# Kernel optimization log

Hardware: AMD Instinct MI355X
Metric: run time of the kernel (lower is better)

The kernel has to match this reference:

```python
import jax, jax.numpy as jnp
import numpy as np


def setup_inputs() -> dict:
    key = jax.random.key(0)
    k1, = jax.random.split(key, 1)
    inputs = jax.random.normal(k1, (16, 64, 64, 512), dtype=jnp.float32)
    gamma = jnp.zeros((1,), dtype=jnp.float32)
    return {"inputs": inputs, "gamma": gamma}


def reference(inputs, gamma):
    # inputs: [B, H, W, C] (NHWC)
    B, H, W, C = inputs.shape
    vec_a = inputs.reshape(B, H * W, C)              # [B, N, C], N = H*W
    # channel Gram matrix: aTa[b, i, j] = sum_n a[b, n, i] * a[b, n, j]
    aTa = jnp.einsum('bni,bnj->bij', vec_a, vec_a)    # [B, C, C]
    attn = jax.nn.softmax(aTa, axis=-1)               # softmax over last axis
    # aaTa = attn @ vec_a^T -> [B, C, N]; transpose -> [B, N, C]
    aaTa = jnp.einsum('bij,bnj->bni', attn, vec_a)    # [B, N, C]
    aaTa = aaTa.reshape(B, H, W, C)
    return gamma * aaTa + inputs
```

## Files before the change

kernel.cpp:

```cpp
#include <hip/hip_runtime.h>

#define BATCH 16
#define NPIX  4096
#define CCH   512
#define NSPLIT 8
#define KSPL  (NPIX / NSPLIT)
#define NUT   10

using bf16x8   = __attribute__((ext_vector_type(8))) __bf16;
using floatx4  = __attribute__((ext_vector_type(4))) float;
using ushort8v = __attribute__((ext_vector_type(8))) unsigned short;
using ushort4v = __attribute__((ext_vector_type(4))) unsigned short;

static __device__ __forceinline__ unsigned short f2bf(float f) {
    unsigned u = __builtin_bit_cast(unsigned, f);
    unsigned r = 0x7fffu + ((u >> 16) & 1u);
    return (unsigned short)((u + r) >> 16);
}
static __device__ __forceinline__ float bf2f(unsigned short v) {
    unsigned u = ((unsigned)v) << 16;
    return __builtin_bit_cast(float, u);
}
static __device__ __forceinline__ void gld16(const unsigned short* g, unsigned short* l) {
    __builtin_amdgcn_global_load_lds(
        (const __attribute__((address_space(1))) void*)g,
        (__attribute__((address_space(3))) void*)l,
        16, 0, 0);
}
#define LOFF(p) ((unsigned)(unsigned long long)(__attribute__((address_space(3))) const void*)(p))
#define DSR(d, a, o) asm volatile("ds_read_b128 %0, %1 offset:" o : "=v"(d) : "v"(a))

__global__ __launch_bounds__(256) void k_cvt(const float* __restrict__ inp,
                                             unsigned short* __restrict__ Abf,
                                             unsigned short* __restrict__ AT) {
    __shared__ unsigned short sN[64 * 66];
    const int bn = blockIdx.x, bc = blockIdx.y, b = blockIdx.z;
    const int t  = threadIdx.x;
    const int n0 = bn * 64, c0 = bc * 64;
    const float* ip = inp + ((size_t)b * NPIX + n0) * CCH + c0;
    unsigned short* op = Abf + ((size_t)b * NPIX + n0) * CCH + c0;

#pragma unroll
    for (int r = 0; r < 2; ++r) {
        int n  = r * 32 + (t >> 3);
        int c8 = (t & 7) * 8;
        float4 v0 = *(const float4*)(ip + (size_t)n * CCH + c8);
        float4 v1 = *(const float4*)(ip + (size_t)n * CCH + c8 + 4);
        ushort8v w;
        w[0] = f2bf(v0.x); w[1] = f2bf(v0.y); w[2] = f2bf(v0.z); w[3] = f2bf(v0.w);
        w[4] = f2bf(v1.x); w[5] = f2bf(v1.y); w[6] = f2bf(v1.z); w[7] = f2bf(v1.w);
        *(ushort8v*)(op + (size_t)n * CCH + c8) = w;
        *(ushort8v*)&sN[n * 66 + c8] = w;
    }
    __syncthreads();

    const int cp = t >> 3;
    const int ng = (t & 7) * 8;
    ushort8v o0, o1;
#pragma unroll
    for (int k = 0; k < 8; ++k) {
        unsigned d = *(const unsigned*)&sN[(ng + k) * 66 + cp * 2];
        o0[k] = (unsigned short)(d & 0xffffu);
        o1[k] = (unsigned short)(d >> 16);
    }
    unsigned short* tp = AT + ((size_t)b * CCH + c0) * NPIX + n0;
    *(ushort8v*)(tp + (size_t)(cp * 2)     * NPIX + ng) = o0;
    *(ushort8v*)(tp + (size_t)(cp * 2 + 1) * NPIX + ng) = o1;
}

#define GEMM_COMP(AADR, BADR)                                                  \
    {                                                                          \
        bf16x8 af[2], bv[8];                                                   \
        DSR(af[0], (AADR), "0");    DSR(af[1], (AADR), "1024");                \
        DSR(bv[0], (BADR), "0");    DSR(bv[1], (BADR), "1024");                \
        DSR(bv[2], (BADR), "2048"); DSR(bv[3], (BADR), "3072");                \
        DSR(bv[4], (BADR), "4096"); DSR(bv[5], (BADR), "5120");                \
        DSR(bv[6], (BADR), "6144"); DSR(bv[7], (BADR), "7168");                \
        asm volatile("s_waitcnt lgkmcnt(0)" ::: "memory");                     \
        __builtin_amdgcn_sched_barrier(0);                                     \
        _Pragma("unroll")                                                      \
        for (int tm = 0; tm < 2; ++tm)                                         \
            _Pragma("unroll")                                                  \
            for (int tn = 0; tn < 8; ++tn)                                     \
                acc[tm][tn] = __builtin_amdgcn_mfma_f32_16x16x32_bf16(         \
                    af[tm], bv[tn], acc[tm][tn], 0, 0, 0);                     \
    }

#define GEMM_WAIT4                                                             \
    asm volatile("s_waitcnt vmcnt(4)" ::: "memory");                           \
    __builtin_amdgcn_s_barrier();
#define GEMM_WAIT0                                                             \
    asm volatile("s_waitcnt vmcnt(0)" ::: "memory");                           \
    __builtin_amdgcn_s_barrier();

__global__ __launch_bounds__(256) void k_ata(const unsigned short* __restrict__ AT,
                                             unsigned short* __restrict__ Sp) {
    __shared__ unsigned short sA0[128 * 32];
    __shared__ unsigned short sA1[128 * 32];
    __shared__ unsigned short sA2[128 * 32];
    __shared__ unsigned short sB0[128 * 32];
    __shared__ unsigned short sB1[128 * 32];
    __shared__ unsigned short sB2[128 * 32];
    const int u = blockIdx.x, s = blockIdx.y, b = blockIdx.z;
    const int ti = (u < 4) ? 0 : (u < 7) ? 1 : (u < 9) ? 2 : 3;
    const int u0 = ti * 5 - (ti * (ti + 1)) / 2;
    const int tj = ti + (u - u0);
    const unsigned short* pa = AT + ((size_t)b * CCH + ti * 128) * NPIX + s * KSPL;
    const unsigned short* pb = AT + ((size_t)b * CCH + tj * 128) * NPIX + s * KSPL;
    const int tid = threadIdx.x, lane = tid & 63, wave = tid >> 6;
    const int lrow = lane >> 2;
    const int lk   = (lane & 3) * 8;
    const int kq   = (lane >> 4) * 8;

    const unsigned aoff = (unsigned)((wave * 32 + (lane & 15)) * 64 + kq * 2);
    const unsigned boff = (unsigned)((lane & 15) * 64 + kq * 2);
    const unsigned aA0 = LOFF(sA0) + aoff, aA1 = LOFF(sA1) + aoff, aA2 = LOFF(sA2) + aoff;
    const unsigned aB0 = LOFF(sB0) + boff, aB1 = LOFF(sB1) + boff, aB2 = LOFF(sB2) + boff;

    floatx4 acc[2][8];
#pragma unroll
    for (int tm = 0; tm < 2; ++tm)
#pragma unroll
        for (int tn = 0; tn < 8; ++tn)
            acc[tm][tn] = floatx4{0.f, 0.f, 0.f, 0.f};

#define STG(DA, DB, K0)                                                        \
    {                                                                          \
        _Pragma("unroll")                                                      \
        for (int i = 0; i < 2; ++i) {                                          \
            const int r = wave * 32 + i * 16;                                  \
            gld16(pa + (size_t)(r + lrow) * NPIX + (K0) + lk, &DA[r * 32]);    \
            gld16(pb + (size_t)(r + lrow) * NPIX + (K0) + lk, &DB[r * 32]);    \
        }                                                                      \
    }
#define BODYS(NA, NB, K2, CA, CB) STG(NA, NB, K2) GEMM_COMP(CA, CB) GEMM_WAIT4

    STG(sA0, sB0, 0)
    STG(sA1, sB1, 32)
    GEMM_WAIT4

    BODYS(sA2, sB2,  64, aA0, aB0)
    BODYS(sA0, sB0,  96, aA1, aB1)
    BODYS(sA1, sB1, 128, aA2, aB2)
    BODYS(sA2, sB2, 160, aA0, aB0)
    BODYS(sA0, sB0, 192, aA1, aB1)
    BODYS(sA1, sB1, 224, aA2, aB2)
    BODYS(sA2, sB2, 256, aA0, aB0)
    BODYS(sA0, sB0, 288, aA1, aB1)
    BODYS(sA1, sB1, 320, aA2, aB2)
    BODYS(sA2, sB2, 352, aA0, aB0)
    BODYS(sA0, sB0, 384, aA1, aB1)
    BODYS(sA1, sB1, 416, aA2, aB2)
    BODYS(sA2, sB2, 448, aA0, aB0)
    BODYS(sA0, sB0, 480, aA1, aB1)
    GEMM_COMP(aA2, aB2) GEMM_WAIT0
    GEMM_COMP(aA0, aB0)
#undef BODYS
#undef STG

    unsigned short* Tb = Sp + ((((size_t)s * BATCH + b) * NUT + u) << 14);
#pragma unroll
    for (int tm = 0; tm < 2; ++tm)
#pragma unroll
        for (int tn = 0; tn < 8; ++tn) {
            ushort4v w;
#pragma unroll
            for (int r = 0; r < 4; ++r) w[r] = f2bf(acc[tm][tn][r]);
            *(ushort4v*)&Tb[((((wave * 2 + tm) * 8 + tn) * 64) + lane) * 4] = w;
        }
}

__global__ __launch_bounds__(256) void k_softmax(const unsigned short* __restrict__ Sp,
                                                 unsigned short* __restrict__ P) {
    __shared__ float red[6];
    const int row = blockIdx.x;
    const int b = row >> 9, i = row & 511;
    const int tid = threadIdx.x, lane = tid & 63, wave = tid >> 6;
    const size_t sstr = (size_t)BATCH * NUT * 16384;

    float x[2];
#pragma unroll
    for (int e = 0; e < 2; ++e) {
        const int j  = tid + e * 256;
        const int ti = i >> 7, tj = j >> 7;
        const int il = i & 127, jl = j & 127;
        const bool sw = ti > tj;
        const int a  = sw ? tj : ti;
        const int cm = sw ? ti : tj;
        const int u  = a * 4 + cm - ((a * (a + 1)) >> 1);
        const int rr = sw ? jl : il;
        const int cc = sw ? il : jl;
        const int off = ((((rr >> 4) * 8 + (cc >> 4)) * 64) +
                         ((rr >> 2) & 3) * 16 + (cc & 15)) * 4 + (rr & 3);
        const size_t base = (((size_t)b * NUT + u) << 14) + off;
        float v = 0.f;
#pragma unroll
        for (int s = 0; s < NSPLIT; ++s) v += bf2f(Sp[base + s * sstr]);
        x[e] = v;
    }

    float m = fmaxf(x[0], x[1]);
#pragma unroll
    for (int o = 32; o; o >>= 1) m = fmaxf(m, __shfl_xor(m, o, 64));
    if (lane == 0) red[wave] = m;
    __syncthreads();
    if (tid == 0) red[4] = fmaxf(fmaxf(red[0], red[1]), fmaxf(red[2], red[3]));
    __syncthreads();
    m = red[4];

    float e0 = __expf(x[0] - m), e1 = __expf(x[1] - m);
    float sum = e0 + e1;
#pragma unroll
    for (int o = 32; o; o >>= 1) sum += __shfl_xor(sum, o, 64);
    if (lane == 0) red[wave] = sum;
    __syncthreads();
    if (tid == 0) red[5] = red[0] + red[1] + red[2] + red[3];
    __syncthreads();
    float inv = 1.0f / red[5];

    P[(size_t)row * CCH + tid]       = f2bf(e0 * inv);
    P[(size_t)row * CCH + tid + 256] = f2bf(e1 * inv);
}

__global__ __launch_bounds__(512) void k_av(const unsigned short* __restrict__ Abf,
                                            const unsigned short* __restrict__ P,
                                            const float* __restrict__ inp,
                                            const float* __restrict__ gamma,
                                            float* __restrict__ out) {
    __shared__ unsigned short sA0[256 * 32];
    __shared__ unsigned short sA1[256 * 32];
    __shared__ unsigned short sA2[256 * 32];
    __shared__ unsigned short sB0[256 * 32];
    __shared__ unsigned short sB1[256 * 32];
    __shared__ unsigned short sB2[256 * 32];
    const int bn = blockIdx.x, bi = blockIdx.y, b = blockIdx.z;
    const unsigned short* pa = Abf + ((size_t)b * NPIX + bn * 256) * CCH;
    const unsigned short* pb = P + ((size_t)b * CCH + bi * 256) * CCH;
    const int tid = threadIdx.x, lane = tid & 63, wave = tid >> 6;
    const int wr = wave >> 2;
    const int wc = wave & 3;
    const int lrow = lane >> 2;
    const int lk   = (lane & 3) * 8;
    const int kq   = (lane >> 4) * 8;
    const float g = gamma[0];

    const unsigned aoff = (unsigned)((wr * 128 + (lane & 15)) * 64 + kq * 2);
    const unsigned boff = (unsigned)((wc * 64 + (lane & 15)) * 64 + kq * 2);
    const unsigned aA0 = LOFF(sA0) + aoff, aA1 = LOFF(sA1) + aoff, aA2 = LOFF(sA2) + aoff;
    const unsigned aB0 = LOFF(sB0) + boff, aB1 = LOFF(sB1) + boff, aB2 = LOFF(sB2) + boff;

    floatx4 acc[8][4];
#pragma unroll
    for (int m = 0; m < 8; ++m)
#pragma unroll
        for (int n = 0; n < 4; ++n)
            acc[m][n] = floatx4{0.f, 0.f, 0.f, 0.f};

#define STG(DA, DB, K0)                                                        \
    {                                                                          \
        _Pragma("unroll")                                                      \
        for (int i = 0; i < 2; ++i) {                                          \
            const int r = (wave * 2 + i) * 16;                                 \
            gld16(pa + (size_t)(r + lrow) * CCH + (K0) + lk, &DA[r * 32]);     \
            gld16(pb + (size_t)(r + lrow) * CCH + (K0) + lk, &DB[r * 32]);     \
        }                                                                      \
    }
#define AV_COMP(AADR, BADR)                                                    \
    {                                                                          \
        bf16x8 af[8], bv[4];                                                   \
        DSR(af[0], (AADR), "0");    DSR(af[1], (AADR), "1024");                \
        DSR(af[2], (AADR), "2048"); DSR(af[3], (AADR), "3072");                \
        DSR(af[4], (AADR), "4096"); DSR(af[5], (AADR), "5120");                \
        DSR(af[6], (AADR), "6144"); DSR(af[7], (AADR), "7168");                \
        DSR(bv[0], (BADR), "0");    DSR(bv[1], (BADR), "1024");                \
        DSR(bv[2], (BADR), "2048"); DSR(bv[3], (BADR), "3072");                \
        asm volatile("s_waitcnt lgkmcnt(0)" ::: "memory");                     \
        __builtin_amdgcn_sched_barrier(0);                                     \
        _Pragma("unroll")                                                      \
        for (int m = 0; m < 8; ++m)                                            \
            _Pragma("unroll")                                                  \
            for (int n = 0; n < 4; ++n)                                        \
                acc[m][n] = __builtin_amdgcn_mfma_f32_16x16x32_bf16(           \
                    af[m], bv[n], acc[m][n], 0, 0, 0);                         \
    }
#define BODYS(NA, NB, K2, CA, CB) STG(NA, NB, K2) AV_COMP(CA, CB) GEMM_WAIT4

    STG(sA0, sB0, 0)
    STG(sA1, sB1, 32)
    GEMM_WAIT4

    BODYS(sA2, sB2,  64, aA0, aB0)
    BODYS(sA0, sB0,  96, aA1, aB1)
    BODYS(sA1, sB1, 128, aA2, aB2)
    BODYS(sA2, sB2, 160, aA0, aB0)
    BODYS(sA0, sB0, 192, aA1, aB1)
    BODYS(sA1, sB1, 224, aA2, aB2)
    BODYS(sA2, sB2, 256, aA0, aB0)
    BODYS(sA0, sB0, 288, aA1, aB1)
    BODYS(sA1, sB1, 320, aA2, aB2)
    BODYS(sA2, sB2, 352, aA0, aB0)
    BODYS(sA0, sB0, 384, aA1, aB1)
    BODYS(sA1, sB1, 416, aA2, aB2)
    BODYS(sA2, sB2, 448, aA0, aB0)
    BODYS(sA0, sB0, 480, aA1, aB1)
    AV_COMP(aA2, aB2) GEMM_WAIT0
    AV_COMP(aA0, aB0)
#undef BODYS
#undef AV_COMP
#undef STG

    float* Ob = out + ((size_t)b * NPIX + bn * 256) * CCH + bi * 256;
    const float* Ib = inp + ((size_t)b * NPIX + bn * 256) * CCH + bi * 256;
#pragma unroll
    for (int m = 0; m < 8; ++m)
#pragma unroll
        for (int n = 0; n < 4; ++n)
#pragma unroll
            for (int r = 0; r < 4; ++r) {
                int nrow = wr * 128 + m * 16 + (lane >> 4) * 4 + r;
                int icol = wc * 64 + n * 16 + (lane & 15);
                size_t o = (size_t)nrow * CCH + icol;
                Ob[o] = g * acc[m][n][r] + Ib[o];
            }
}

extern "C" void kernel_launch(void* const* d_in, const int* in_sizes, int n_in,
                              void* d_out, int out_size, void* d_ws, size_t ws_size,
                              hipStream_t stream) {
    const float* inp   = (const float*)d_in[0];
    const float* gamma = (const float*)d_in[1];
    float* out = (float*)d_out;

    char* ws = (char*)d_ws;
    unsigned short* Abf = (unsigned short*)ws;
    unsigned short* AT  = (unsigned short*)(ws + (size_t)67108864);
    unsigned short* Sp  = (unsigned short*)(ws + (size_t)134217728);
    unsigned short* P   = (unsigned short*)(ws + (size_t)134217728 + 41943040);

    k_cvt<<<dim3(NPIX / 64, CCH / 64, BATCH), 256, 0, stream>>>(inp, Abf, AT);
    k_ata<<<dim3(NUT, NSPLIT, BATCH), 256, 0, stream>>>(AT, Sp);
    k_softmax<<<BATCH * CCH, 256, 0, stream>>>(Sp, P);
    k_av<<<dim3(NPIX / 256, CCH / 256, BATCH), 512, 0, stream>>>(Abf, P, inp, gamma, out);
}
```

Baseline: 394.5 us.

## Process four softmax rows per block and shrink AV pipeline to double buffer

```diff
diff --git a/kernel.cpp b/kernel.cpp
--- a/kernel.cpp
+++ b/kernel.cpp
@@ -172,54 +172,82 @@
 
 __global__ __launch_bounds__(256) void k_softmax(const unsigned short* __restrict__ Sp,
                                                  unsigned short* __restrict__ P) {
-    __shared__ float red[6];
-    const int row = blockIdx.x;
-    const int b = row >> 9, i = row & 511;
+    __shared__ float red[4][4];
+    const int blk = blockIdx.x;
+    const int b = blk >> 7, r0 = blk & 127;
+    const int i4  = r0 * 4;
+    const int ti  = i4 >> 7;
+    const int il0 = i4 & 127;
     const int tid = threadIdx.x, lane = tid & 63, wave = tid >> 6;
     const size_t sstr = (size_t)BATCH * NUT * 16384;
 
-    float x[2];
+    float x[2][4];
+#pragma unroll
+    for (int e = 0; e < 2; ++e)
+#pragma unroll
+        for (int k = 0; k < 4; ++k) x[e][k] = 0.f;
+
 #pragma unroll
     for (int e = 0; e < 2; ++e) {
         const int j  = tid + e * 256;
-        const int ti = i >> 7, tj = j >> 7;
-        const int il = i & 127, jl = j & 127;
-        const bool sw = ti > tj;
-        const int a  = sw ? tj : ti;
-        const int cm = sw ? ti : tj;
-        const int u  = a * 4 + cm - ((a * (a + 1)) >> 1);
-        const int rr = sw ? jl : il;
-        const int cc = sw ? il : jl;
-        const int off = ((((rr >> 4) * 8 + (cc >> 4)) * 64) +
-                         ((rr >> 2) & 3) * 16 + (cc & 15)) * 4 + (rr & 3);
-        const size_t base = (((size_t)b * NUT + u) << 14) + off;
-        float v = 0.f;
-#pragma unroll
-        for (int s = 0; s < NSPLIT; ++s) v += bf2f(Sp[base + s * sstr]);
-        x[e] = v;
-    }
-
-    float m = fmaxf(x[0], x[1]);
-#pragma unroll
-    for (int o = 32; o; o >>= 1) m = fmaxf(m, __shfl_xor(m, o, 64));
-    if (lane == 0) red[wave] = m;
+        const int tj = j >> 7, jl = j & 127;
+        if (ti <= tj) {
+            const int u = ti * 4 + tj - ((ti * (ti + 1)) >> 1);
+            const int off = (((il0 >> 4) * 8 + (jl >> 4)) * 64 +
+                             ((il0 >> 2) & 3) * 16 + (jl & 15)) * 4;
+            const size_t base = (((size_t)b * NUT + u) << 14) + off;
+#pragma unroll
+            for (int s = 0; s < NSPLIT; ++s) {
+                ushort4v v = *(const ushort4v*)&Sp[base + s * sstr];
+                x[e][0] += bf2f(v[0]); x[e][1] += bf2f(v[1]);
+                x[e][2] += bf2f(v[2]); x[e][3] += bf2f(v[3]);
+            }
+        } else {
+            const int u = tj * 4 + ti - ((tj * (tj + 1)) >> 1);
+            const int off = ((((jl >> 4) * 8 + (il0 >> 4)) * 64 +
+                              ((jl >> 2) & 3) * 16 + (il0 & 15)) * 4) + (jl & 3);
+            const size_t base = (((size_t)b * NUT + u) << 14) + off;
+#pragma unroll
+            for (int s = 0; s < NSPLIT; ++s) {
+                const unsigned short* p = &Sp[base + s * sstr];
+                x[e][0] += bf2f(p[0]);  x[e][1] += bf2f(p[4]);
+                x[e][2] += bf2f(p[8]);  x[e][3] += bf2f(p[12]);
+            }
+        }
+    }
+
+#pragma unroll
+    for (int k = 0; k < 4; ++k) {
+        float m = fmaxf(x[0][k], x[1][k]);
+#pragma unroll
+        for (int o = 32; o; o >>= 1) m = fmaxf(m, __shfl_xor(m, o, 64));
+        if (lane == 0) red[wave][k] = m;
+    }
     __syncthreads();
-    if (tid == 0) red[4] = fmaxf(fmaxf(red[0], red[1]), fmaxf(red[2], red[3]));
+    float m4[4];
+#pragma unroll
+    for (int k = 0; k < 4; ++k)
+        m4[k] = fmaxf(fmaxf(red[0][k], red[1][k]), fmaxf(red[2][k], red[3][k]));
     __syncthreads();
-    m = red[4];
-
-    float e0 = __expf(x[0] - m), e1 = __expf(x[1] - m);
-    float sum = e0 + e1;
-#pragma unroll
-    for (int o = 32; o; o >>= 1) sum += __shfl_xor(sum, o, 64);
-    if (lane == 0) red[wave] = sum;
+
+    float e0[4], e1[4];
+#pragma unroll
+    for (int k = 0; k < 4; ++k) {
+        e0[k] = __expf(x[0][k] - m4[k]);
+        e1[k] = __expf(x[1][k] - m4[k]);
+        float s = e0[k] + e1[k];
+#pragma unroll
+        for (int o = 32; o; o >>= 1) s += __shfl_xor(s, o, 64);
+        if (lane == 0) red[wave][k] = s;
+    }
     __syncthreads();
-    if (tid == 0) red[5] = red[0] + red[1] + red[2] + red[3];
-    __syncthreads();
-    float inv = 1.0f / red[5];
-
-    P[(size_t)row * CCH + tid]       = f2bf(e0 * inv);
-    P[(size_t)row * CCH + tid + 256] = f2bf(e1 * inv);
+#pragma unroll
+    for (int k = 0; k < 4; ++k) {
+        float inv = 1.0f / (red[0][k] + red[1][k] + red[2][k] + red[3][k]);
+        const size_t rowo = ((size_t)(b * 512 + i4 + k)) * CCH;
+        P[rowo + tid]       = f2bf(e0[k] * inv);
+        P[rowo + tid + 256] = f2bf(e1[k] * inv);
+    }
 }
 
 __global__ __launch_bounds__(512) void k_av(const unsigned short* __restrict__ Abf,
@@ -229,10 +257,8 @@
                                             float* __restrict__ out) {
     __shared__ unsigned short sA0[256 * 32];
     __shared__ unsigned short sA1[256 * 32];
-    __shared__ unsigned short sA2[256 * 32];
     __shared__ unsigned short sB0[256 * 32];
     __shared__ unsigned short sB1[256 * 32];
-    __shared__ unsigned short sB2[256 * 32];
     const int bn = blockIdx.x, bi = blockIdx.y, b = blockIdx.z;
     const unsigned short* pa = Abf + ((size_t)b * NPIX + bn * 256) * CCH;
     const unsigned short* pb = P + ((size_t)b * CCH + bi * 256) * CCH;
@@ -246,8 +272,8 @@
 
     const unsigned aoff = (unsigned)((wr * 128 + (lane & 15)) * 64 + kq * 2);
     const unsigned boff = (unsigned)((wc * 64 + (lane & 15)) * 64 + kq * 2);
-    const unsigned aA0 = LOFF(sA0) + aoff, aA1 = LOFF(sA1) + aoff, aA2 = LOFF(sA2) + aoff;
-    const unsigned aB0 = LOFF(sB0) + boff, aB1 = LOFF(sB1) + boff, aB2 = LOFF(sB2) + boff;
+    const unsigned aA0 = LOFF(sA0) + aoff, aA1 = LOFF(sA1) + aoff;
+    const unsigned aB0 = LOFF(sB0) + boff, aB1 = LOFF(sB1) + boff;
 
     floatx4 acc[8][4];
 #pragma unroll
@@ -283,28 +309,27 @@
                 acc[m][n] = __builtin_amdgcn_mfma_f32_16x16x32_bf16(           \
                     af[m], bv[n], acc[m][n], 0, 0, 0);                         \
     }
-#define BODYS(NA, NB, K2, CA, CB) STG(NA, NB, K2) AV_COMP(CA, CB) GEMM_WAIT4
+#define BODYS(NA, NB, K2, CA, CB) STG(NA, NB, K2) AV_COMP(CA, CB) GEMM_WAIT0
 
     STG(sA0, sB0, 0)
-    STG(sA1, sB1, 32)
-    GEMM_WAIT4
-
-    BODYS(sA2, sB2,  64, aA0, aB0)
-    BODYS(sA0, sB0,  96, aA1, aB1)
-    BODYS(sA1, sB1, 128, aA2, aB2)
-    BODYS(sA2, sB2, 160, aA0, aB0)
+    GEMM_WAIT0
+
+    BODYS(sA1, sB1,  32, aA0, aB0)
+    BODYS(sA0, sB0,  64, aA1, aB1)
+    BODYS(sA1, sB1,  96, aA0, aB0)
+    BODYS(sA0, sB0, 128, aA1, aB1)
+    BODYS(sA1, sB1, 160, aA0, aB0)
     BODYS(sA0, sB0, 192, aA1, aB1)
-    BODYS(sA1, sB1, 224, aA2, aB2)
-    BODYS(sA2, sB2, 256, aA0, aB0)
-    BODYS(sA0, sB0, 288, aA1, aB1)
-    BODYS(sA1, sB1, 320, aA2, aB2)
-    BODYS(sA2, sB2, 352, aA0, aB0)
+    BODYS(sA1, sB1, 224, aA0, aB0)
+    BODYS(sA0, sB0, 256, aA1, aB1)
+    BODYS(sA1, sB1, 288, aA0, aB0)
+    BODYS(sA0, sB0, 320, aA1, aB1)
+    BODYS(sA1, sB1, 352, aA0, aB0)
     BODYS(sA0, sB0, 384, aA1, aB1)
-    BODYS(sA1, sB1, 416, aA2, aB2)
-    BODYS(sA2, sB2, 448, aA0, aB0)
-    BODYS(sA0, sB0, 480, aA1, aB1)
-    AV_COMP(aA2, aB2) GEMM_WAIT0
-    AV_COMP(aA0, aB0)
+    BODYS(sA1, sB1, 416, aA0, aB0)
+    BODYS(sA0, sB0, 448, aA1, aB1)
+    BODYS(sA1, sB1, 480, aA0, aB0)
+    AV_COMP(aA1, aB1)
 #undef BODYS
 #undef AV_COMP
 #undef STG
@@ -339,6 +364,6 @@
 
     k_cvt<<<dim3(NPIX / 64, CCH / 64, BATCH), 256, 0, stream>>>(inp, Abf, AT);
     k_ata<<<dim3(NUT, NSPLIT, BATCH), 256, 0, stream>>>(AT, Sp);
-    k_softmax<<<BATCH * CCH, 256, 0, stream>>>(Sp, P);
+    k_softmax<<<BATCH * 128, 256, 0, stream>>>(Sp, P);
     k_av<<<dim3(NPIX / 256, CCH / 256, BATCH), 512, 0, stream>>>(Abf, P, inp, gamma, out);
 }
```

Result: faster. 380.9 us (-3.4%).
